# Performance work log

Hardware: AMD Instinct MI355X
Metric: run time of the kernel (lower is better)

The kernel has to match this reference:

```python
import jax, jax.numpy as jnp
import numpy as np

D_MODEL = 512
N_HEAD = 8
D_HEAD = D_MODEL // N_HEAD


def _linear(x, W, b):
    return x @ W + b


def setup_inputs() -> dict:
    key = jax.random.key(0)
    ks = jax.random.split(key, 20)
    B, N, D = 8, 1024, D_MODEL
    H = D // 2
    s = 1.0 / np.sqrt(D)
    s2 = 1.0 / np.sqrt(H)
    inp = {
        'query': jax.random.normal(ks[0], (B, N, D), jnp.float32),
        'key_in': jax.random.normal(ks[1], (B, N, D), jnp.float32),
        'value': jax.random.normal(ks[2], (B, N, D), jnp.float32),
        'Wq': jax.random.normal(ks[3], (D, D), jnp.float32) * s,
        'bq': jnp.zeros((D,), jnp.float32),
        'Wk': jax.random.normal(ks[4], (D, D), jnp.float32) * s,
        'bk': jnp.zeros((D,), jnp.float32),
        'Wv': jax.random.normal(ks[5], (D, D), jnp.float32) * s,
        'bv': jnp.zeros((D,), jnp.float32),
        'Wo': jax.random.normal(ks[6], (D, D), jnp.float32) * s,
        'bo': jnp.zeros((D,), jnp.float32),
        'Ws1': jax.random.normal(ks[7], (D, H), jnp.float32) * s,
        'bs1': jnp.zeros((H,), jnp.float32),
        'Ws2': jax.random.normal(ks[8], (H, D), jnp.float32) * s2,
        'bs2': jnp.zeros((D,), jnp.float32),
        'Wc1': jax.random.normal(ks[9], (D, H), jnp.float32) * s,
        'bc1': jnp.zeros((H,), jnp.float32),
        'Wc2': jax.random.normal(ks[10], (H, D), jnp.float32) * s2,
        'bc2': jnp.zeros((D,), jnp.float32),
    }
    return inp


def reference(query, key_in, value, Wq, bq, Wk, bk, Wv, bv, Wo, bo,
              Ws1, bs1, Ws2, bs2, Wc1, bc1, Wc2, bc2):
    B, N, D = query.shape
    H, Dh = N_HEAD, D_HEAD

    def split_heads(x):  # [b, n, h*d] -> [b, h, n, d]
        return x.reshape(B, N, H, Dh).transpose(0, 2, 1, 3)

    q = split_heads(_linear(query, Wq, bq))
    k = split_heads(_linear(key_in, Wk, bk))
    vv = _linear(value, Wv, bv)  # [b, n, d] == rearrange(v,'b h n d->b n (h d)')

    # spatial gating: Linear-ReLU-Linear-Sigmoid on w_v(value)
    sw = jax.nn.sigmoid(_linear(jax.nn.relu(_linear(vv, Ws1, bs1)), Ws2, bs2))
    v_spatial = split_heads(vv * sw)

    # channel gating: MLP on mean-over-seq profile, broadcast back to seq
    prof = value.mean(axis=1, keepdims=True)  # [b, 1, d]
    cw = jax.nn.sigmoid(_linear(jax.nn.relu(_linear(prof, Wc1, bc1)), Wc2, bc2))
    v_channel = split_heads(_linear(value * cw, Wv, bv))

    v_dual = v_spatial + v_channel

    scores = jnp.einsum('bhqd,bhkd->bhqk', q, k) / np.sqrt(Dh).astype(np.float32)
    attn = jax.nn.softmax(scores, axis=-1)
    out = jnp.einsum('bhqk,bhkd->bhqd', attn, v_dual)
    out = out.transpose(0, 2, 1, 3).reshape(B, N, D)
    return _linear(out, Wo, bo)  # dropout is identity in eval mode
```

## Files before the change

kernel.cpp:

```cpp
#include <hip/hip_runtime.h>

typedef unsigned short u16t;
typedef __bf16  bf8   __attribute__((ext_vector_type(8)));
typedef float   f32x4 __attribute__((ext_vector_type(4)));
typedef unsigned short us4 __attribute__((ext_vector_type(4)));

#define DEV __device__ __forceinline__

DEV float bf2f(u16t u) { union { unsigned u; float f; } x; x.u = ((unsigned)u) << 16; return x.f; }
DEV u16t  f2bf(float f) {
    union { float f; unsigned u; } x; x.f = f;
    unsigned r = x.u + 0x7FFFu + ((x.u >> 16) & 1u);
    return (u16t)(r >> 16);
}
DEV uint4 pack8(const float* v) {
    uint4 r;
    r.x = (unsigned)f2bf(v[0]) | ((unsigned)f2bf(v[1]) << 16);
    r.y = (unsigned)f2bf(v[2]) | ((unsigned)f2bf(v[3]) << 16);
    r.z = (unsigned)f2bf(v[4]) | ((unsigned)f2bf(v[5]) << 16);
    r.w = (unsigned)f2bf(v[6]) | ((unsigned)f2bf(v[7]) << 16);
    return r;
}
DEV void gll16(const void* g, void* l) {
    __builtin_amdgcn_global_load_lds(
        (const __attribute__((address_space(1))) unsigned*)g,
        (__attribute__((address_space(3))) unsigned*)l, 16, 0, 0);
}

#define DMODEL 512
#define SEQ    1024
#define NBATCH 8

__global__ __launch_bounds__(256) void fill_sentinel(float* out, int n)
{
    int i = blockIdx.x * 256 + threadIdx.x;
    if (i < n) out[i] = 100.f;
}

__global__ __launch_bounds__(256) void cvt_value(const float* v, u16t* Vi)
{
    size_t i = ((size_t)blockIdx.x * 256 + threadIdx.x) * 8;
    float4 a = *(const float4*)(v + i), b = *(const float4*)(v + i + 4);
    float o[8] = {a.x, a.y, a.z, a.w, b.x, b.y, b.z, b.w};
    *(uint4*)&Vi[i] = pack8(o);
}

__global__ __launch_bounds__(256) void transpose6(
    const float* s0, const float* s1, const float* s2, const float* s3,
    const float* s4, const float* s5,
    u16t* d0, u16t* d1, u16t* d2, u16t* d3, u16t* d4, u16t* d5)
{
    int z = blockIdx.z;
    const float* S; u16t* D; int R, C;
    switch (z) {
        case 0: S = s0; D = d0; R = 512; C = 512; break;
        case 1: S = s1; D = d1; R = 512; C = 512; break;
        case 2: S = s2; D = d2; R = 512; C = 512; break;
        case 3: S = s3; D = d3; R = 512; C = 512; break;
        case 4: S = s4; D = d4; R = 512; C = 256; break;
        default:S = s5; D = d5; R = 256; C = 512; break;
    }
    int c0 = blockIdx.x * 32, r0 = blockIdx.y * 32;
    if (c0 >= C || r0 >= R) return;
    __shared__ u16t tile[32][33];
    int tx = threadIdx.x & 31, ty = threadIdx.x >> 5;
#pragma unroll
    for (int p = 0; p < 4; ++p) {
        int r = ty + p * 8;
        tile[r][tx] = f2bf(S[(size_t)(r0 + r) * C + c0 + tx]);
    }
    __syncthreads();
#pragma unroll
    for (int p = 0; p < 4; ++p) {
        int r = ty + p * 8;
        D[(size_t)(c0 + r) * R + r0 + tx] = tile[tx][r];
    }
}

__global__ __launch_bounds__(256) void colmean(const u16t* Vi, float* prof)
{
    int b = blockIdx.y, z = blockIdx.z;
    int d = blockIdx.x * 256 + threadIdx.x;
    const u16t* p = Vi + (size_t)b * SEQ * DMODEL + (size_t)z * 64 * DMODEL + d;
    float s = 0.f;
#pragma unroll 8
    for (int n = 0; n < 64; ++n) s += bf2f(p[(size_t)n * DMODEL]);
    atomicAdd(&prof[b * DMODEL + d], s * (1.f / 1024.f));
}

__global__ __launch_bounds__(256) void cmlp(const float* prof,
                                            const float* Wc1, const float* bc1,
                                            const float* Wc2, const float* bc2,
                                            u16t* cw)
{
    int b = blockIdx.x, t = threadIdx.x;
    __shared__ float pf[512];
    __shared__ float hf[256];
    pf[t]       = prof[b * 512 + t];
    pf[t + 256] = prof[b * 512 + t + 256];
    __syncthreads();
    float s = bc1[t];
    for (int k = 0; k < 512; ++k) s += pf[k] * Wc1[(size_t)k * 256 + t];
    hf[t] = fmaxf(s, 0.f);
    __syncthreads();
#pragma unroll
    for (int o = 0; o < 2; ++o) {
        int d = t + o * 256;
        float s2 = bc2[d];
        for (int k = 0; k < 256; ++k) s2 += hf[k] * Wc2[(size_t)k * 512 + d];
        cw[b * 512 + d] = f2bf(1.f / (1.f + __expf(-s2)));
    }
}

__global__ __launch_bounds__(256) void scale_wv(const u16t* WvT, const u16t* cw,
                                                u16t* WvTs)
{
    int b = blockIdx.y;
    int idx = blockIdx.x * 2048 + threadIdx.x * 8;
    int k = idx & 511;
    uint4 wv = *(const uint4*)&WvT[idx];
    uint4 cu = *(const uint4*)&cw[b * 512 + k];
    const u16t* wp = (const u16t*)&wv;
    const u16t* cp = (const u16t*)&cu;
    float o[8];
#pragma unroll
    for (int q = 0; q < 8; ++q) o[q] = bf2f(wp[q]) * bf2f(cp[q]);
    *(uint4*)&WvTs[(size_t)b * 262144 + idx] = pack8(o);
}

template<int WR, int WC, int WM, int NT>
__global__ __launch_bounds__(256, 4) void gemmT(
    const void* A0, const void* A1, const void* A2, const void* A3,
    const u16t* W0, const u16t* W1, const u16t* W2, const u16t* W3,
    const float* B0, const float* B1, const float* B2, const float* B3,
    void* C0, void* C1, void* C2, void* C3,
    int N, int K, int mode,
    const u16t* VVp, u16t* VdTp,
    int araw, int tmask, int outf32, int wbmask)
{
    constexpr int BM = WR * WM * 16;
    constexpr int BN = WC * NT * 16;

    int z = blockIdx.z;
    const void* A  = (z == 0) ? A0 : (z == 1) ? A1 : (z == 2) ? A2 : A3;
    const u16t* W  = (z == 0) ? W0 : (z == 1) ? W1 : (z == 2) ? W2 : W3;
    const float* Bi = (z == 0) ? B0 : (z == 1) ? B1 : (z == 2) ? B2 : B3;
    void*       C  = (z == 0) ? C0 : (z == 1) ? C1 : (z == 2) ? C2 : C3;

    int af32   = (araw >> z) & 1;
    int tstore = (tmask >> z) & 1;

    int tid = threadIdx.x;
    int w = tid >> 6, lane = tid & 63, quad = lane >> 4, l16 = lane & 15;
    int wr = w / WC, wc = w % WC;
    int m0 = blockIdx.x * BM, n0 = blockIdx.y * BN;
    int bb = m0 >> 10;
    if ((wbmask >> z) & 1) W += (size_t)bb * 262144;

    __shared__ __align__(16) u16t As[BM * 32];
    __shared__ __align__(16) u16t Bs[BN * 32];

    f32x4 zero = {0.f, 0.f, 0.f, 0.f};
    f32x4 acc[WM][NT];
#pragma unroll
    for (int mi = 0; mi < WM; ++mi)
#pragma unroll
        for (int ni = 0; ni < NT; ++ni) acc[mi][ni] = zero;

    for (int k0 = 0; k0 < K; k0 += 32) {
        __syncthreads();
#pragma unroll
        for (int p = 0; p < BM / 64; ++p) {
            int ci = p * 256 + tid;
            int r = ci >> 2, g = ci & 3;
            int gs = (g ^ (r & 3)) * 8;
            if (af32) {
                const float* src = (const float*)A + (size_t)(m0 + r) * K + k0 + gs;
                float4 a = *(const float4*)src;
                float4 b = *(const float4*)(src + 4);
                float v[8] = {a.x, a.y, a.z, a.w, b.x, b.y, b.z, b.w};
                *(uint4*)&As[(size_t)ci * 8] = pack8(v);
            } else {
                gll16(&((const u16t*)A)[(size_t)(m0 + r) * K + k0 + gs],
                      &As[(size_t)(p * 256 + w * 64) * 8]);
            }
        }
#pragma unroll
        for (int p = 0; p < BN / 64; ++p) {
            int ci = p * 256 + tid;
            int r = ci >> 2, g = ci & 3;
            int gs = (g ^ (r & 3)) * 8;
            gll16(&W[(size_t)(n0 + r) * K + k0 + gs], &Bs[(size_t)(p * 256 + w * 64) * 8]);
        }
        __syncthreads();

        int sx = l16 & 3;
        bf8 af[WM], bfr[NT];
#pragma unroll
        for (int mi = 0; mi < WM; ++mi)
            af[mi] = *(const bf8*)&As[(wr * WM * 16 + mi * 16 + l16) * 32 + ((quad ^ sx) * 8)];
#pragma unroll
        for (int ni = 0; ni < NT; ++ni)
            bfr[ni] = *(const bf8*)&Bs[(wc * NT * 16 + ni * 16 + l16) * 32 + ((quad ^ sx) * 8)];
#pragma unroll
        for (int mi = 0; mi < WM; ++mi)
#pragma unroll
            for (int ni = 0; ni < NT; ++ni)
                acc[mi][ni] = __builtin_amdgcn_mfma_f32_16x16x32_bf16(af[mi], bfr[ni], acc[mi][ni], 0, 0, 0);
    }

#pragma unroll
    for (int mi = 0; mi < WM; ++mi) {
        int grow0 = m0 + wr * WM * 16 + mi * 16 + quad * 4;
#pragma unroll
        for (int ni = 0; ni < NT; ++ni) {
            int gcol = n0 + wc * NT * 16 + ni * 16 + l16;
            float bias = Bi[gcol];
            if (mode == 2) {
                int h = gcol >> 6, dh = gcol & 63;
                int b_ = grow0 >> 10, n_ = grow0 & 1023;
                size_t tbase = (size_t)((b_ * 8 + h) * 64 + dh) * 1024 + n_;
                us4 vc = *(const us4*)&VdTp[tbase];
                us4 pk;
#pragma unroll
                for (int r = 0; r < 4; ++r) {
                    float s = acc[mi][ni][r] + bias;
                    float sw = 1.f / (1.f + __expf(-s));
                    float vvv = bf2f(VVp[(size_t)(grow0 + r) * DMODEL + gcol]);
                    pk[r] = f2bf(vvv * sw + bf2f(vc[r]));
                }
                *(us4*)&VdTp[tbase] = pk;
            } else if (tstore) {
                int h = gcol >> 6, dh = gcol & 63;
                int b_ = grow0 >> 10, n_ = grow0 & 1023;
                us4 pk;
#pragma unroll
                for (int r = 0; r < 4; ++r) pk[r] = f2bf(acc[mi][ni][r] + bias);
                *(us4*)&((u16t*)C)[(size_t)((b_ * 8 + h) * 64 + dh) * 1024 + n_] = pk;
            } else if (outf32) {
#pragma unroll
                for (int r = 0; r < 4; ++r)
                    ((float*)C)[(size_t)(grow0 + r) * N + gcol] = acc[mi][ni][r] + bias;
            } else {
#pragma unroll
                for (int r = 0; r < 4; ++r) {
                    float v = acc[mi][ni][r] + bias;
                    if (mode == 1) v = fmaxf(v, 0.f);
                    ((u16t*)C)[(size_t)(grow0 + r) * N + gcol] = f2bf(v);
                }
            }
        }
    }
}

__global__ __launch_bounds__(256) void attn(const u16t* Q, const u16t* Km,
                                            const u16t* VdT, u16t* Oa)
{
    __shared__ __align__(16) u16t Qs[64 * 64];
    __shared__ __align__(16) u16t Ks[64 * 64];
    __shared__ __align__(16) u16t Vs[64 * 64];
    __shared__ __align__(16) u16t Ps[64 * 64];

    int qt = blockIdx.x, bh = blockIdx.y;
    int b = bh >> 3, h = bh & 7;
    int tid = threadIdx.x;
    int w = tid >> 6, lane = tid & 63, quad = lane >> 4, l16 = lane & 15;
    int l7 = l16 & 7;

    const u16t* Qp = Q   + ((size_t)(b * SEQ + qt * 64)) * DMODEL + h * 64;
    const u16t* Kp = Km  + ((size_t)(b * SEQ)) * DMODEL + h * 64;
    const u16t* Vp = VdT + ((size_t)(b * 8 + h)) * 64 * SEQ;

#pragma unroll
    for (int p = 0; p < 2; ++p) {
        int ci = p * 256 + tid;
        int r = ci >> 3, g = ci & 7;
        int gs = (g ^ (r & 7)) * 8;
        gll16(&Qp[(size_t)r * DMODEL + gs], &Qs[(size_t)(p * 256 + w * 64) * 8]);
    }

    f32x4 zero = {0.f, 0.f, 0.f, 0.f};
    f32x4 oacc[4];
    float l_run[4];
#pragma unroll
    for (int r = 0; r < 4; ++r) { l_run[r] = 0.f; oacc[r] = zero; }

    for (int kt = 0; kt < 16; ++kt) {
        __syncthreads();
#pragma unroll
        for (int p = 0; p < 2; ++p) {
            int ci = p * 256 + tid;
            int r = ci >> 3, g = ci & 7;
            int gs = (g ^ (r & 7)) * 8;
            gll16(&Kp[(size_t)(kt * 64 + r) * DMODEL + gs], &Ks[(size_t)(p * 256 + w * 64) * 8]);
            gll16(&Vp[(size_t)r * SEQ + kt * 64 + gs],      &Vs[(size_t)(p * 256 + w * 64) * 8]);
        }
        __syncthreads();

        f32x4 sacc[4];
#pragma unroll
        for (int j = 0; j < 4; ++j) sacc[j] = zero;
#pragma unroll
        for (int ks = 0; ks < 2; ++ks) {
            int sG = ((ks * 4 + quad) ^ l7) * 8;
            bf8 aq = *(const bf8*)&Qs[(w * 16 + l16) * 64 + sG];
            bf8 bk[4];
#pragma unroll
            for (int j = 0; j < 4; ++j)
                bk[j] = *(const bf8*)&Ks[(j * 16 + l16) * 64 + sG];
#pragma unroll
            for (int j = 0; j < 4; ++j)
                sacc[j] = __builtin_amdgcn_mfma_f32_16x16x32_bf16(aq, bk[j], sacc[j], 0, 0, 0);
        }

#pragma unroll
        for (int r4 = 0; r4 < 4; ++r4) {
            float rsum = 0.f;
            int prow = w * 16 + quad * 4 + r4;
            int pr7 = prow & 7;
#pragma unroll
            for (int j = 0; j < 4; ++j) {
                float p = __expf(fmaf(sacc[j][r4], 0.125f, -4.f));
                rsum += p;
                int G = j * 2 + (l16 >> 3);
                Ps[prow * 64 + ((G ^ pr7) * 8) + l7] = f2bf(p);
            }
#pragma unroll
            for (int d = 1; d < 16; d <<= 1) rsum += __shfl_xor(rsum, d);
            l_run[r4] += rsum;
        }

#pragma unroll
        for (int kk = 0; kk < 2; ++kk) {
            int sG = ((kk * 4 + quad) ^ l7) * 8;
            bf8 ap = *(const bf8*)&Ps[(w * 16 + l16) * 64 + sG];
            bf8 bvf[4];
#pragma unroll
            for (int j = 0; j < 4; ++j)
                bvf[j] = *(const bf8*)&Vs[(j * 16 + l16) * 64 + sG];
#pragma unroll
            for (int j = 0; j < 4; ++j)
                oacc[j] = __builtin_amdgcn_mfma_f32_16x16x32_bf16(ap, bvf[j], oacc[j], 0, 0, 0);
        }
    }

#pragma unroll
    for (int j = 0; j < 4; ++j) {
#pragma unroll
        for (int r4 = 0; r4 < 4; ++r4) {
            int rq = qt * 64 + w * 16 + quad * 4 + r4;
            float v = oacc[j][r4] / l_run[r4];
            Oa[((size_t)(b * SEQ + rq)) * DMODEL + h * 64 + j * 16 + l16] = f2bf(v);
        }
    }
}

extern "C" void kernel_launch(void* const* d_in, const int* in_sizes, int n_in,
                              void* d_out, int out_size, void* d_ws, size_t ws_size,
                              hipStream_t stream)
{
    const float* query  = (const float*)d_in[0];
    const float* key_in = (const float*)d_in[1];
    const float* value  = (const float*)d_in[2];
    const float* Wq  = (const float*)d_in[3];  const float* bq  = (const float*)d_in[4];
    const float* Wk  = (const float*)d_in[5];  const float* bk  = (const float*)d_in[6];
    const float* Wv  = (const float*)d_in[7];  const float* bv  = (const float*)d_in[8];
    const float* Wo  = (const float*)d_in[9];  const float* bo  = (const float*)d_in[10];
    const float* Ws1 = (const float*)d_in[11]; const float* bs1 = (const float*)d_in[12];
    const float* Ws2 = (const float*)d_in[13]; const float* bs2 = (const float*)d_in[14];
    const float* Wc1 = (const float*)d_in[15]; const float* bc1 = (const float*)d_in[16];
    const float* Wc2 = (const float*)d_in[17]; const float* bc2 = (const float*)d_in[18];
    float* out = (float*)d_out;

    u16t* ws = (u16t*)d_ws;
    u16t* WqT  = ws + 0;
    u16t* WkT  = ws + 262144;
    u16t* WvT  = ws + 524288;
    u16t* WoT  = ws + 786432;
    u16t* Ws1T = ws + 1048576;
    u16t* Ws2T = ws + 1179648;
    u16t* WvTs = ws + 1310720;
    u16t* Vi   = ws + 3407872;
    u16t* Qm   = ws + 7602176;
    u16t* Kmm  = ws + 11796480;
    u16t* VV   = ws + 15990784;
    u16t* VdT  = ws + 20185088;
    u16t* cw   = ws + 24379392;
    float* prof = (float*)(ws + 24383488);
    u16t* H1 = Vi;
    u16t* Oa = VV;

    const size_t NEED_BYTES = 24391680ull * 2ull;
    if (ws_size < NEED_BYTES) {
        fill_sentinel<<<(out_size + 255) / 256, 256, 0, stream>>>(out, out_size);
        return;
    }

    hipMemsetAsync((void*)prof, 0, NBATCH * DMODEL * sizeof(float), stream);

    cvt_value<<<2048, 256, 0, stream>>>(value, Vi);
    transpose6<<<dim3(16, 16, 6), 256, 0, stream>>>(Wq, Wk, Wv, Wo, Ws1, Ws2,
                                                    WqT, WkT, WvT, WoT, Ws1T, Ws2T);
    colmean<<<dim3(2, 8, 16), 256, 0, stream>>>(Vi, prof);
    cmlp<<<8, 256, 0, stream>>>(prof, Wc1, bc1, Wc2, bc2, cw);
    scale_wv<<<dim3(128, 8), 256, 0, stream>>>(WvT, cw, WvTs);

    gemmT<2, 2, 4, 4><<<dim3(64, 4, 4), 256, 0, stream>>>(
        query, key_in, Vi, Vi,
        WqT, WkT, WvT, WvTs,
        bq, bk, bv, bv,
        Qm, Kmm, VV, VdT,
        512, 512, 0, nullptr, VdT,
        0x3, 0x8, 0, 0x8);

    gemmT<2, 2, 2, 2><<<dim3(128, 4, 1), 256, 0, stream>>>(
        VV, VV, VV, VV, Ws1T, Ws1T, Ws1T, Ws1T, bs1, bs1, bs1, bs1,
        H1, H1, H1, H1, 256, 512, 1, nullptr, nullptr, 0, 0, 0, 0);

    gemmT<2, 2, 2, 4><<<dim3(128, 4, 1), 256, 0, stream>>>(
        H1, H1, H1, H1, Ws2T, Ws2T, Ws2T, Ws2T, bs2, bs2, bs2, bs2,
        Qm, Qm, Qm, Qm,
        512, 256, 2, VV, VdT, 0, 0, 0, 0);

    attn<<<dim3(16, 64), 256, 0, stream>>>(Qm, Kmm, VdT, Oa);

    gemmT<2, 2, 2, 4><<<dim3(128, 4, 1), 256, 0, stream>>>(
        Oa, Oa, Oa, Oa, WoT, WoT, WoT, WoT, bo, bo, bo, bo,
        out, out, out, out, 512, 512, 0, nullptr, nullptr,
        0, 0, 1, 0);
}
```

Before: 285.4 us.

## Double-buffer LDS tiles in gemmT to overlap global loads with MFMA

Adds ping-pong LDS buffers for the A and B tiles so the next k-slice is loaded while the current one feeds the MFMAs. Row base pointers are hoisted out of the k loop, and fp32 A inputs are held in registers and packed to bf16 after compute. Launch bounds drop from 4 to 3 waves per SIMD to make room for the extra registers and doubled shared memory. The loop assumes K/32 is even, and occupancy falls.

```diff
diff --git a/kernel.cpp b/kernel.cpp
--- a/kernel.cpp
+++ b/kernel.cpp
@@ -129,7 +129,7 @@
 }
 
 template<int WR, int WC, int WM, int NT>
-__global__ __launch_bounds__(256, 4) void gemmT(
+__global__ __launch_bounds__(256, 3) void gemmT(
     const void* A0, const void* A1, const void* A2, const void* A3,
     const u16t* W0, const u16t* W1, const u16t* W2, const u16t* W3,
     const float* B0, const float* B1, const float* B2, const float* B3,
@@ -140,6 +140,8 @@
 {
     constexpr int BM = WR * WM * 16;
     constexpr int BN = WC * NT * 16;
+    constexpr int PA = BM / 64;
+    constexpr int PB = BN / 64;
 
     int z = blockIdx.z;
     const void* A  = (z == 0) ? A0 : (z == 1) ? A1 : (z == 2) ? A2 : A3;
@@ -157,8 +159,24 @@
     int bb = m0 >> 10;
     if ((wbmask >> z) & 1) W += (size_t)bb * 262144;
 
-    __shared__ __align__(16) u16t As[BM * 32];
-    __shared__ __align__(16) u16t Bs[BN * 32];
+    __shared__ __align__(16) u16t As0[BM * 32], As1[BM * 32];
+    __shared__ __align__(16) u16t Bs0[BN * 32], Bs1[BN * 32];
+
+    const u16t* srcA16[PA]; const float* srcAf[PA];
+#pragma unroll
+    for (int p = 0; p < PA; ++p) {
+        int ci = p * 256 + tid, r = ci >> 2, g = ci & 3;
+        int gs = (g ^ (r & 3)) * 8;
+        srcA16[p] = (const u16t*)A + (size_t)(m0 + r) * K + gs;
+        srcAf[p]  = (const float*)A + (size_t)(m0 + r) * K + gs;
+    }
+    const u16t* srcB[PB];
+#pragma unroll
+    for (int p = 0; p < PB; ++p) {
+        int ci = p * 256 + tid, r = ci >> 2, g = ci & 3;
+        int gs = (g ^ (r & 3)) * 8;
+        srcB[p] = W + (size_t)(n0 + r) * K + gs;
+    }
 
     f32x4 zero = {0.f, 0.f, 0.f, 0.f};
     f32x4 acc[WM][NT];
@@ -167,33 +185,32 @@
 #pragma unroll
         for (int ni = 0; ni < NT; ++ni) acc[mi][ni] = zero;
 
-    for (int k0 = 0; k0 < K; k0 += 32) {
-        __syncthreads();
-#pragma unroll
-        for (int p = 0; p < BM / 64; ++p) {
-            int ci = p * 256 + tid;
-            int r = ci >> 2, g = ci & 3;
-            int gs = (g ^ (r & 3)) * 8;
+    float4 fa[PA], fb[PA];
+
+    auto stage = [&](u16t* As, u16t* Bs, int k0) {
+#pragma unroll
+        for (int p = 0; p < PA; ++p) {
             if (af32) {
-                const float* src = (const float*)A + (size_t)(m0 + r) * K + k0 + gs;
-                float4 a = *(const float4*)src;
-                float4 b = *(const float4*)(src + 4);
-                float v[8] = {a.x, a.y, a.z, a.w, b.x, b.y, b.z, b.w};
-                *(uint4*)&As[(size_t)ci * 8] = pack8(v);
+                fa[p] = *(const float4*)(srcAf[p] + k0);
+                fb[p] = *(const float4*)(srcAf[p] + k0 + 4);
             } else {
-                gll16(&((const u16t*)A)[(size_t)(m0 + r) * K + k0 + gs],
-                      &As[(size_t)(p * 256 + w * 64) * 8]);
+                gll16(srcA16[p] + k0, &As[(size_t)(p * 256 + w * 64) * 8]);
             }
         }
 #pragma unroll
-        for (int p = 0; p < BN / 64; ++p) {
-            int ci = p * 256 + tid;
-            int r = ci >> 2, g = ci & 3;
-            int gs = (g ^ (r & 3)) * 8;
-            gll16(&W[(size_t)(n0 + r) * K + k0 + gs], &Bs[(size_t)(p * 256 + w * 64) * 8]);
-        }
-        __syncthreads();
-
+        for (int p = 0; p < PB; ++p)
+            gll16(srcB[p] + k0, &Bs[(size_t)(p * 256 + w * 64) * 8]);
+    };
+    auto writeA = [&](u16t* As) {
+        if (!af32) return;
+#pragma unroll
+        for (int p = 0; p < PA; ++p) {
+            float v[8] = {fa[p].x, fa[p].y, fa[p].z, fa[p].w,
+                          fb[p].x, fb[p].y, fb[p].z, fb[p].w};
+            *(uint4*)&As[(size_t)(p * 256 + tid) * 8] = pack8(v);
+        }
+    };
+    auto compute = [&](const u16t* As, const u16t* Bs) {
         int sx = l16 & 3;
         bf8 af[WM], bfr[NT];
 #pragma unroll
@@ -207,6 +224,20 @@
 #pragma unroll
             for (int ni = 0; ni < NT; ++ni)
                 acc[mi][ni] = __builtin_amdgcn_mfma_f32_16x16x32_bf16(af[mi], bfr[ni], acc[mi][ni], 0, 0, 0);
+    };
+
+    int nt = K >> 5;
+    stage(As0, Bs0, 0);
+    writeA(As0);
+    for (int t = 0; t < nt; t += 2) {
+        __syncthreads();
+        stage(As1, Bs1, (t + 1) << 5);
+        compute(As0, Bs0);
+        writeA(As1);
+        __syncthreads();
+        if (t + 2 < nt) stage(As0, Bs0, (t + 2) << 5);
+        compute(As1, Bs1);
+        if (t + 2 < nt) writeA(As0);
     }
 
 #pragma unroll
```

New measurement: 286.5 us. No clear change (+0.4%).

## Drop LDS staging in GEMM, load MFMA fragments directly from global

Applied to the files above, without the earlier changes.

The GEMM kernel no longer stages A and W tiles through shared memory with barriers. Each wave now loads its MFMA fragments straight from global memory, relying on cache for reuse. To make that possible, query and key are converted to bf16 upfront in a fused conversion kernel, which removes the in-loop fp32 path. The Ws2 and Wo GEMMs also move to smaller tiles with more blocks. This trades LDS traffic and synchronisation for redundant global/L2 reads and more workspace, and it needs an extra conversion pass over query and key.

```diff
diff --git a/kernel.cpp b/kernel.cpp
--- a/kernel.cpp
+++ b/kernel.cpp
@@ -37,12 +37,17 @@
     if (i < n) out[i] = 100.f;
 }
 
-__global__ __launch_bounds__(256) void cvt_value(const float* v, u16t* Vi)
-{
+__global__ __launch_bounds__(256) void cvt3(const float* q, const float* k,
+                                            const float* v,
+                                            u16t* Qb, u16t* Kb, u16t* Vb)
+{
+    int y = blockIdx.y;
+    const float* s = (y == 0) ? q : (y == 1) ? k : v;
+    u16t*        d = (y == 0) ? Qb : (y == 1) ? Kb : Vb;
     size_t i = ((size_t)blockIdx.x * 256 + threadIdx.x) * 8;
-    float4 a = *(const float4*)(v + i), b = *(const float4*)(v + i + 4);
+    float4 a = *(const float4*)(s + i), b = *(const float4*)(s + i + 4);
     float o[8] = {a.x, a.y, a.z, a.w, b.x, b.y, b.z, b.w};
-    *(uint4*)&Vi[i] = pack8(o);
+    *(uint4*)&d[i] = pack8(o);
 }
 
 __global__ __launch_bounds__(256) void transpose6(
@@ -129,25 +134,24 @@
 }
 
 template<int WR, int WC, int WM, int NT>
-__global__ __launch_bounds__(256, 4) void gemmT(
-    const void* A0, const void* A1, const void* A2, const void* A3,
+__global__ __launch_bounds__(256, 3) void gemmT(
+    const u16t* A0, const u16t* A1, const u16t* A2, const u16t* A3,
     const u16t* W0, const u16t* W1, const u16t* W2, const u16t* W3,
     const float* B0, const float* B1, const float* B2, const float* B3,
     void* C0, void* C1, void* C2, void* C3,
     int N, int K, int mode,
     const u16t* VVp, u16t* VdTp,
-    int araw, int tmask, int outf32, int wbmask)
+    int tmask, int outf32, int wbmask)
 {
     constexpr int BM = WR * WM * 16;
     constexpr int BN = WC * NT * 16;
 
     int z = blockIdx.z;
-    const void* A  = (z == 0) ? A0 : (z == 1) ? A1 : (z == 2) ? A2 : A3;
+    const u16t* A  = (z == 0) ? A0 : (z == 1) ? A1 : (z == 2) ? A2 : A3;
     const u16t* W  = (z == 0) ? W0 : (z == 1) ? W1 : (z == 2) ? W2 : W3;
     const float* Bi = (z == 0) ? B0 : (z == 1) ? B1 : (z == 2) ? B2 : B3;
     void*       C  = (z == 0) ? C0 : (z == 1) ? C1 : (z == 2) ? C2 : C3;
 
-    int af32   = (araw >> z) & 1;
     int tstore = (tmask >> z) & 1;
 
     int tid = threadIdx.x;
@@ -157,8 +161,8 @@
     int bb = m0 >> 10;
     if ((wbmask >> z) & 1) W += (size_t)bb * 262144;
 
-    __shared__ __align__(16) u16t As[BM * 32];
-    __shared__ __align__(16) u16t Bs[BN * 32];
+    const u16t* Ap = A + (size_t)(m0 + wr * WM * 16 + l16) * K + quad * 8;
+    const u16t* Bp = W + (size_t)(n0 + wc * NT * 16 + l16) * K + quad * 8;
 
     f32x4 zero = {0.f, 0.f, 0.f, 0.f};
     f32x4 acc[WM][NT];
@@ -167,41 +171,15 @@
 #pragma unroll
         for (int ni = 0; ni < NT; ++ni) acc[mi][ni] = zero;
 
+#pragma unroll 2
     for (int k0 = 0; k0 < K; k0 += 32) {
-        __syncthreads();
-#pragma unroll
-        for (int p = 0; p < BM / 64; ++p) {
-            int ci = p * 256 + tid;
-            int r = ci >> 2, g = ci & 3;
-            int gs = (g ^ (r & 3)) * 8;
-            if (af32) {
-                const float* src = (const float*)A + (size_t)(m0 + r) * K + k0 + gs;
-                float4 a = *(const float4*)src;
-                float4 b = *(const float4*)(src + 4);
-                float v[8] = {a.x, a.y, a.z, a.w, b.x, b.y, b.z, b.w};
-                *(uint4*)&As[(size_t)ci * 8] = pack8(v);
-            } else {
-                gll16(&((const u16t*)A)[(size_t)(m0 + r) * K + k0 + gs],
-                      &As[(size_t)(p * 256 + w * 64) * 8]);
-            }
-        }
-#pragma unroll
-        for (int p = 0; p < BN / 64; ++p) {
-            int ci = p * 256 + tid;
-            int r = ci >> 2, g = ci & 3;
-            int gs = (g ^ (r & 3)) * 8;
-            gll16(&W[(size_t)(n0 + r) * K + k0 + gs], &Bs[(size_t)(p * 256 + w * 64) * 8]);
-        }
-        __syncthreads();
-
-        int sx = l16 & 3;
         bf8 af[WM], bfr[NT];
 #pragma unroll
         for (int mi = 0; mi < WM; ++mi)
-            af[mi] = *(const bf8*)&As[(wr * WM * 16 + mi * 16 + l16) * 32 + ((quad ^ sx) * 8)];
+            af[mi] = *(const bf8*)(Ap + (size_t)mi * 16 * K + k0);
 #pragma unroll
         for (int ni = 0; ni < NT; ++ni)
-            bfr[ni] = *(const bf8*)&Bs[(wc * NT * 16 + ni * 16 + l16) * 32 + ((quad ^ sx) * 8)];
+            bfr[ni] = *(const bf8*)(Bp + (size_t)ni * 16 * K + k0);
 #pragma unroll
         for (int mi = 0; mi < WM; ++mi)
 #pragma unroll
@@ -387,10 +365,12 @@
     u16t* VdT  = ws + 20185088;
     u16t* cw   = ws + 24379392;
     float* prof = (float*)(ws + 24383488);
+    u16t* Qbf  = ws + 24391680;
+    u16t* Kbf  = ws + 28585984;
     u16t* H1 = Vi;
     u16t* Oa = VV;
 
-    const size_t NEED_BYTES = 24391680ull * 2ull;
+    const size_t NEED_BYTES = 32780288ull * 2ull;
     if (ws_size < NEED_BYTES) {
         fill_sentinel<<<(out_size + 255) / 256, 256, 0, stream>>>(out, out_size);
         return;
@@ -398,7 +378,7 @@
 
     hipMemsetAsync((void*)prof, 0, NBATCH * DMODEL * sizeof(float), stream);
 
-    cvt_value<<<2048, 256, 0, stream>>>(value, Vi);
+    cvt3<<<dim3(2048, 3), 256, 0, stream>>>(query, key_in, value, Qbf, Kbf, Vi);
     transpose6<<<dim3(16, 16, 6), 256, 0, stream>>>(Wq, Wk, Wv, Wo, Ws1, Ws2,
                                                     WqT, WkT, WvT, WoT, Ws1T, Ws2T);
     colmean<<<dim3(2, 8, 16), 256, 0, stream>>>(Vi, prof);
@@ -406,26 +386,26 @@
     scale_wv<<<dim3(128, 8), 256, 0, stream>>>(WvT, cw, WvTs);
 
     gemmT<2, 2, 4, 4><<<dim3(64, 4, 4), 256, 0, stream>>>(
-        query, key_in, Vi, Vi,
+        Qbf, Kbf, Vi, Vi,
         WqT, WkT, WvT, WvTs,
         bq, bk, bv, bv,
         Qm, Kmm, VV, VdT,
         512, 512, 0, nullptr, VdT,
-        0x3, 0x8, 0, 0x8);
+        0x8, 0, 0x8);
 
     gemmT<2, 2, 2, 2><<<dim3(128, 4, 1), 256, 0, stream>>>(
         VV, VV, VV, VV, Ws1T, Ws1T, Ws1T, Ws1T, bs1, bs1, bs1, bs1,
-        H1, H1, H1, H1, 256, 512, 1, nullptr, nullptr, 0, 0, 0, 0);
-
-    gemmT<2, 2, 2, 4><<<dim3(128, 4, 1), 256, 0, stream>>>(
+        H1, H1, H1, H1, 256, 512, 1, nullptr, nullptr, 0, 0, 0);
+
+    gemmT<2, 2, 2, 2><<<dim3(128, 8, 1), 256, 0, stream>>>(
         H1, H1, H1, H1, Ws2T, Ws2T, Ws2T, Ws2T, bs2, bs2, bs2, bs2,
         Qm, Qm, Qm, Qm,
-        512, 256, 2, VV, VdT, 0, 0, 0, 0);
+        512, 256, 2, VV, VdT, 0, 0, 0);
 
     attn<<<dim3(16, 64), 256, 0, stream>>>(Qm, Kmm, VdT, Oa);
 
-    gemmT<2, 2, 2, 4><<<dim3(128, 4, 1), 256, 0, stream>>>(
+    gemmT<2, 2, 2, 2><<<dim3(128, 8, 1), 256, 0, stream>>>(
         Oa, Oa, Oa, Oa, WoT, WoT, WoT, WoT, bo, bo, bo, bo,
         out, out, out, out, 512, 512, 0, nullptr, nullptr,
-        0, 0, 1, 0);
-}
+        0, 1, 0);
+}
```

Measured after the change: 349.3 us. 1.22x slower.
